# Performance work log

Hardware: AMD Instinct MI355X
Metric: run time of the kernel (lower is better)

Reference implementation:

```python
import jax, jax.numpy as jnp
import numpy as np

IN_F = 4096
OUT_F = 4096
Q_LEVELS = 16  # 4-bit


def setup_inputs() -> dict:
    key = jax.random.key(0)
    k = jax.random.split(key, 7)
    input = jax.random.normal(k[0], (4, 128, IN_F), dtype=jnp.float32)
    qweight = jax.random.randint(k[1], (OUT_F, IN_F), 0, Q_LEVELS, dtype=jnp.int32)
    scales = jax.random.uniform(k[2], (OUT_F, 1), dtype=jnp.float32)
    zeros = jax.random.uniform(k[3], (OUT_F, 1), dtype=jnp.float32)
    outlier = jax.random.uniform(k[4], (OUT_F, IN_F), dtype=jnp.float32)
    grad_updates = jax.random.normal(k[5], (OUT_F, IN_F), dtype=jnp.float32)
    bias = jax.random.normal(k[6], (OUT_F,), dtype=jnp.float32)
    return {"input": input, "qweight": qweight, "scales": scales,
            "zeros": zeros, "outlier": outlier,
            "grad_updates": grad_updates, "bias": bias}


def reference(input, qweight, scales, zeros, outlier, grad_updates, bias):
    # dequantize: affine per-output-row quantization -> dense weight [out, in]
    weight = (qweight.astype(jnp.float32) - zeros) * scales
    # sparse outlier correction (densified), scaled by learned GradUpdates
    weight = weight + outlier * grad_updates
    # F.linear: y = x @ W^T + b
    return jnp.einsum('bsi,oi->bso', input, weight) + bias
```

## Files before the change

kernel.cpp:

```cpp
#include <hip/hip_runtime.h>
#include <stdint.h>

#define IN_F   4096
#define OUT_F  4096
#define M_TOT  512
#define KT     (IN_F / 32)
#define BN     64
#define BK     64
#define KSPLIT 4
#define KPB    (IN_F / KSPLIT)
#define NITER  (KPB / BK)

typedef unsigned short u16;
typedef __bf16 bf16x8 __attribute__((ext_vector_type(8)));
typedef float  f32x4  __attribute__((ext_vector_type(4)));
typedef int    i32x4  __attribute__((ext_vector_type(4)));
typedef float  fv4    __attribute__((ext_vector_type(4)));

__device__ __forceinline__ u16 f2bf(float x) {
    unsigned u = __float_as_uint(x);
    u += 0x7FFFu + ((u >> 16) & 1u);
    return (u16)(u >> 16);
}

__global__ void pack_a_kernel(const float* __restrict__ in, u16* __restrict__ aws) {
    int t    = blockIdx.x * blockDim.x + threadIdx.x;
    int lane = t & 63;
    int kt   = (t >> 6) & (KT - 1);
    int mt   = t >> 13;
    int m = mt * 16 + (lane & 15);
    int k = kt * 32 + ((lane >> 4) << 3);
    const float* src = in + (size_t)m * IN_F + k;
    float4 a0 = *(const float4*)src;
    float4 a1 = *(const float4*)(src + 4);
    union { u16 u[8]; uint4 v; } pk;
    pk.u[0]=f2bf(a0.x); pk.u[1]=f2bf(a0.y); pk.u[2]=f2bf(a0.z); pk.u[3]=f2bf(a0.w);
    pk.u[4]=f2bf(a1.x); pk.u[5]=f2bf(a1.y); pk.u[6]=f2bf(a1.z); pk.u[7]=f2bf(a1.w);
    *(uint4*)(aws + (size_t)t * 8) = pk.v;
}

__global__ __launch_bounds__(1024, 4) void qlinear_kernel(
    const u16*   __restrict__ aws,
    const int*   __restrict__ qw,
    const float* __restrict__ scales,
    const float* __restrict__ zeros,
    const float* __restrict__ outlier,
    const float* __restrict__ grad,
    float*       __restrict__ part)
{
    __shared__ __align__(16) u16 Bsh[2][8 * 64 * 8];

    const int tid  = threadIdx.x;
    const int lane = tid & 63;
    const int wv   = tid >> 6;

    const int nblk = blockIdx.x >> 2;
    const int kq   = blockIdx.x & 3;
    const int n0   = nblk * BN;
    const int k0   = kq * KPB;

    const int srow = tid >> 4;
    const int schk = tid & 15;
    const int orow = n0 + srow;
    const float sr = scales[orow];
    const float c0 = -zeros[orow] * sr;
    const size_t sg = (size_t)orow * IN_F + k0 + schk * 4;
    const int sks   = schk >> 3;
    const int squad = (schk >> 1) & 3;
    const int j0    = (schk & 1) * 4;
    const int snf   = srow >> 4;
    const int slane = (srow & 15) | (squad << 4);
    const int doff  = ((sks * 4 + snf) * 64 + slane) * 8 + j0;

    i32x4 qb[2]; fv4 ob[2], gb[2];
    auto ld = [&](int it) {
        int s = it & 1;
        size_t off = sg + (size_t)it * BK;
        qb[s] = __builtin_nontemporal_load((const i32x4*)(qw      + off));
        ob[s] = __builtin_nontemporal_load((const fv4*)  (outlier + off));
        gb[s] = __builtin_nontemporal_load((const fv4*)  (grad    + off));
    };
    auto st = [&](int it) {
        int s = it & 1;
        union { u16 u[4]; uint2 v; } pk;
        pk.u[0] = f2bf(fmaf((float)qb[s].x, sr, fmaf(ob[s].x, gb[s].x, c0)));
        pk.u[1] = f2bf(fmaf((float)qb[s].y, sr, fmaf(ob[s].y, gb[s].y, c0)));
        pk.u[2] = f2bf(fmaf((float)qb[s].z, sr, fmaf(ob[s].z, gb[s].z, c0)));
        pk.u[3] = f2bf(fmaf((float)qb[s].w, sr, fmaf(ob[s].w, gb[s].w, c0)));
        *(uint2*)(&Bsh[it & 1][doff]) = pk.v;
    };

    const u16* abase = aws + ((size_t)(wv * 2) * KT + kq * (KPB / 32)) * 512
                           + (size_t)lane * 8;

    f32x4 acc[2][4] = {};

    ld(0);
    ld(1);
    st(0);
    asm volatile("s_waitcnt lgkmcnt(0)" ::: "memory");
    __builtin_amdgcn_s_barrier();

    for (int it = 0; it < NITER; ++it) {
        bf16x8 af[2][2];
        #pragma unroll
        for (int ks = 0; ks < 2; ++ks)
            #pragma unroll
            for (int mf = 0; mf < 2; ++mf)
                af[ks][mf] = *(const bf16x8*)(abase + ((size_t)mf * KT + it * 2 + ks) * 512);

        if (it + 2 < NITER) ld(it + 2);

        const u16* bb = &Bsh[it & 1][0];
        #pragma unroll
        for (int ks = 0; ks < 2; ++ks) {
            bf16x8 bfr[4];
            #pragma unroll
            for (int nf = 0; nf < 4; ++nf)
                bfr[nf] = *(const bf16x8*)(bb + (((ks * 4 + nf) * 64) + lane) * 8);
            #pragma unroll
            for (int mf = 0; mf < 2; ++mf)
                #pragma unroll
                for (int nf = 0; nf < 4; ++nf)
                    acc[mf][nf] = __builtin_amdgcn_mfma_f32_16x16x32_bf16(
                        af[ks][mf], bfr[nf], acc[mf][nf], 0, 0, 0);
        }

        if (it + 1 < NITER) st(it + 1);

        asm volatile("s_waitcnt lgkmcnt(0)" ::: "memory");
        __builtin_amdgcn_s_barrier();
    }

    float* pout = part + (size_t)kq * (M_TOT * OUT_F);
    const int cm0 = wv * 32 + ((lane >> 4) << 2);
    const int cn  = n0 + (lane & 15);
    #pragma unroll
    for (int mf = 0; mf < 2; ++mf)
        #pragma unroll
        for (int nf = 0; nf < 4; ++nf)
            #pragma unroll
            for (int r = 0; r < 4; ++r)
                __builtin_nontemporal_store(
                    acc[mf][nf][r],
                    pout + (size_t)(cm0 + mf * 16 + r) * OUT_F + cn + nf * 16);
}

__global__ void reduce_kernel(const fv4* __restrict__ part,
                              const fv4* __restrict__ bias,
                              fv4* __restrict__ out) {
    int idx = blockIdx.x * blockDim.x + threadIdx.x;
    fv4 s = bias[idx & (OUT_F / 4 - 1)];
    const int STRIDE = M_TOT * OUT_F / 4;
    #pragma unroll
    for (int k = 0; k < KSPLIT; ++k) {
        fv4 p = __builtin_nontemporal_load(part + (size_t)k * STRIDE + idx);
        s += p;
    }
    out[idx] = s;
}

extern "C" void kernel_launch(void* const* d_in, const int* in_sizes, int n_in,
                              void* d_out, int out_size, void* d_ws, size_t ws_size,
                              hipStream_t stream) {
    const float* input   = (const float*)d_in[0];
    const int*   qweight = (const int*)  d_in[1];
    const float* scales  = (const float*)d_in[2];
    const float* zeros   = (const float*)d_in[3];
    const float* outlier = (const float*)d_in[4];
    const float* grad    = (const float*)d_in[5];
    const float* bias    = (const float*)d_in[6];
    float* out = (float*)d_out;

    u16*   aws  = (u16*)d_ws;
    float* part = (float*)((char*)d_ws + (4u << 20));

    pack_a_kernel<<<(M_TOT * IN_F / 8) / 256, 256, 0, stream>>>(input, aws);
    qlinear_kernel<<<(OUT_F / BN) * KSPLIT, 1024, 0, stream>>>(
        aws, qweight, scales, zeros, outlier, grad, part);
    reduce_kernel<<<(M_TOT * OUT_F / 4) / 256, 256, 0, stream>>>(
        (const fv4*)part, (const fv4*)bias, (fv4*)out);
}
```

Measured before the change: 215.9 us.

## Halve output tile width to double block count and per-CU occupancy

Reduces the N tile from 64 to 32 columns, doubling the number of blocks and raising the launch-bounds occupancy hint so two blocks can share a CU. The per-thread weight loads shrink to 2-element vectors and the shared-memory B tile and accumulator set halve. The aim is more concurrent waves to hide the latency of the fp32/int32 weight streams. In exchange, each block rereads the full activation slice, doubling A-operand traffic, and loads become narrower.

```diff
diff --git a/kernel.cpp b/kernel.cpp
--- a/kernel.cpp
+++ b/kernel.cpp
@@ -5,7 +5,7 @@
 #define OUT_F  4096
 #define M_TOT  512
 #define KT     (IN_F / 32)
-#define BN     64
+#define BN     32
 #define BK     64
 #define KSPLIT 4
 #define KPB    (IN_F / KSPLIT)
@@ -14,7 +14,8 @@
 typedef unsigned short u16;
 typedef __bf16 bf16x8 __attribute__((ext_vector_type(8)));
 typedef float  f32x4  __attribute__((ext_vector_type(4)));
-typedef int    i32x4  __attribute__((ext_vector_type(4)));
+typedef float  f32x2  __attribute__((ext_vector_type(2)));
+typedef int    i32x2  __attribute__((ext_vector_type(2)));
 typedef float  fv4    __attribute__((ext_vector_type(4)));
 
 __device__ __forceinline__ u16 f2bf(float x) {
@@ -39,7 +40,7 @@
     *(uint4*)(aws + (size_t)t * 8) = pk.v;
 }
 
-__global__ __launch_bounds__(1024, 4) void qlinear_kernel(
+__global__ __launch_bounds__(1024, 8) void qlinear_kernel(
     const u16*   __restrict__ aws,
     const int*   __restrict__ qw,
     const float* __restrict__ scales,
@@ -48,7 +49,7 @@
     const float* __restrict__ grad,
     float*       __restrict__ part)
 {
-    __shared__ __align__(16) u16 Bsh[2][8 * 64 * 8];
+    __shared__ __align__(16) u16 Bsh[2][4 * 64 * 8];
 
     const int tid  = threadIdx.x;
     const int lane = tid & 63;
@@ -59,41 +60,39 @@
     const int n0   = nblk * BN;
     const int k0   = kq * KPB;
 
-    const int srow = tid >> 4;
-    const int schk = tid & 15;
+    const int srow = tid >> 5;
+    const int schk = tid & 31;
     const int orow = n0 + srow;
     const float sr = scales[orow];
     const float c0 = -zeros[orow] * sr;
-    const size_t sg = (size_t)orow * IN_F + k0 + schk * 4;
-    const int sks   = schk >> 3;
-    const int squad = (schk >> 1) & 3;
-    const int j0    = (schk & 1) * 4;
+    const size_t sg = (size_t)orow * IN_F + k0 + schk * 2;
+    const int sks   = schk >> 4;
+    const int squad = (schk >> 2) & 3;
+    const int j0    = (schk & 3) * 2;
     const int snf   = srow >> 4;
     const int slane = (srow & 15) | (squad << 4);
-    const int doff  = ((sks * 4 + snf) * 64 + slane) * 8 + j0;
+    const int doff  = ((sks * 2 + snf) * 64 + slane) * 8 + j0;
 
-    i32x4 qb[2]; fv4 ob[2], gb[2];
+    i32x2 qb[2]; f32x2 ob[2], gb[2];
     auto ld = [&](int it) {
         int s = it & 1;
         size_t off = sg + (size_t)it * BK;
-        qb[s] = __builtin_nontemporal_load((const i32x4*)(qw      + off));
-        ob[s] = __builtin_nontemporal_load((const fv4*)  (outlier + off));
-        gb[s] = __builtin_nontemporal_load((const fv4*)  (grad    + off));
+        qb[s] = __builtin_nontemporal_load((const i32x2*)(qw      + off));
+        ob[s] = __builtin_nontemporal_load((const f32x2*)(outlier + off));
+        gb[s] = __builtin_nontemporal_load((const f32x2*)(grad    + off));
     };
     auto st = [&](int it) {
         int s = it & 1;
-        union { u16 u[4]; uint2 v; } pk;
+        union { u16 u[2]; unsigned v; } pk;
         pk.u[0] = f2bf(fmaf((float)qb[s].x, sr, fmaf(ob[s].x, gb[s].x, c0)));
         pk.u[1] = f2bf(fmaf((float)qb[s].y, sr, fmaf(ob[s].y, gb[s].y, c0)));
-        pk.u[2] = f2bf(fmaf((float)qb[s].z, sr, fmaf(ob[s].z, gb[s].z, c0)));
-        pk.u[3] = f2bf(fmaf((float)qb[s].w, sr, fmaf(ob[s].w, gb[s].w, c0)));
-        *(uint2*)(&Bsh[it & 1][doff]) = pk.v;
+        *(unsigned*)(&Bsh[it & 1][doff]) = pk.v;
     };
 
     const u16* abase = aws + ((size_t)(wv * 2) * KT + kq * (KPB / 32)) * 512
                            + (size_t)lane * 8;
 
-    f32x4 acc[2][4] = {};
+    f32x4 acc[2][2] = {};
 
     ld(0);
     ld(1);
@@ -114,16 +113,12 @@
         const u16* bb = &Bsh[it & 1][0];
         #pragma unroll
         for (int ks = 0; ks < 2; ++ks) {
-            bf16x8 bfr[4];
-            #pragma unroll
-            for (int nf = 0; nf < 4; ++nf)
-                bfr[nf] = *(const bf16x8*)(bb + (((ks * 4 + nf) * 64) + lane) * 8);
-            #pragma unroll
-            for (int mf = 0; mf < 2; ++mf)
-                #pragma unroll
-                for (int nf = 0; nf < 4; ++nf)
-                    acc[mf][nf] = __builtin_amdgcn_mfma_f32_16x16x32_bf16(
-                        af[ks][mf], bfr[nf], acc[mf][nf], 0, 0, 0);
+            bf16x8 bf0 = *(const bf16x8*)(bb + (((ks * 2 + 0) * 64) + lane) * 8);
+            bf16x8 bf1 = *(const bf16x8*)(bb + (((ks * 2 + 1) * 64) + lane) * 8);
+            acc[0][0] = __builtin_amdgcn_mfma_f32_16x16x32_bf16(af[ks][0], bf0, acc[0][0], 0, 0, 0);
+            acc[0][1] = __builtin_amdgcn_mfma_f32_16x16x32_bf16(af[ks][0], bf1, acc[0][1], 0, 0, 0);
+            acc[1][0] = __builtin_amdgcn_mfma_f32_16x16x32_bf16(af[ks][1], bf0, acc[1][0], 0, 0, 0);
+            acc[1][1] = __builtin_amdgcn_mfma_f32_16x16x32_bf16(af[ks][1], bf1, acc[1][1], 0, 0, 0);
         }
 
         if (it + 1 < NITER) st(it + 1);
@@ -138,7 +133,7 @@
     #pragma unroll
     for (int mf = 0; mf < 2; ++mf)
         #pragma unroll
-        for (int nf = 0; nf < 4; ++nf)
+        for (int nf = 0; nf < 2; ++nf)
             #pragma unroll
             for (int r = 0; r < 4; ++r)
                 __builtin_nontemporal_store(
```

After: 257.1 us. +19.1%, slower.

## Split weight dequantization into a separate bf16 pass and swizzle LDS layout

Applied to the files above, without the earlier changes.

Moves the dequantization of qweight, outlier and grad into its own full-occupancy elementwise kernel that writes a bf16 weight buffer to workspace. The GEMM kernel then streams only bf16 weights and stores them directly to LDS. An XOR swizzle on the LDS store and load offsets is added to reduce bank conflicts. This unfuses the dequant from the GEMM, adding a write and re-read of a 32MB bf16 buffer in exchange for better bandwidth saturation in the dequant stage and a lighter GEMM inner loop.

```diff
diff --git a/kernel.cpp b/kernel.cpp
--- a/kernel.cpp
+++ b/kernel.cpp
@@ -39,13 +39,40 @@
     *(uint4*)(aws + (size_t)t * 8) = pk.v;
 }
 
-__global__ __launch_bounds__(1024, 4) void qlinear_kernel(
-    const u16*   __restrict__ aws,
+__global__ __launch_bounds__(256) void dequant_kernel(
     const int*   __restrict__ qw,
     const float* __restrict__ scales,
     const float* __restrict__ zeros,
     const float* __restrict__ outlier,
     const float* __restrict__ grad,
+    u16*         __restrict__ wws)
+{
+    int t = blockIdx.x * blockDim.x + threadIdx.x;
+    int row = t >> 9;
+    const float sr = scales[row];
+    const float c0 = -zeros[row] * sr;
+    size_t e = (size_t)t * 8;
+    i32x4 q0 = __builtin_nontemporal_load((const i32x4*)(qw      + e));
+    i32x4 q1 = __builtin_nontemporal_load((const i32x4*)(qw      + e + 4));
+    fv4   o0 = __builtin_nontemporal_load((const fv4*)  (outlier + e));
+    fv4   o1 = __builtin_nontemporal_load((const fv4*)  (outlier + e + 4));
+    fv4   g0 = __builtin_nontemporal_load((const fv4*)  (grad    + e));
+    fv4   g1 = __builtin_nontemporal_load((const fv4*)  (grad    + e + 4));
+    union { u16 u[8]; uint4 v; } pk;
+    pk.u[0] = f2bf(fmaf((float)q0.x, sr, fmaf(o0.x, g0.x, c0)));
+    pk.u[1] = f2bf(fmaf((float)q0.y, sr, fmaf(o0.y, g0.y, c0)));
+    pk.u[2] = f2bf(fmaf((float)q0.z, sr, fmaf(o0.z, g0.z, c0)));
+    pk.u[3] = f2bf(fmaf((float)q0.w, sr, fmaf(o0.w, g0.w, c0)));
+    pk.u[4] = f2bf(fmaf((float)q1.x, sr, fmaf(o1.x, g1.x, c0)));
+    pk.u[5] = f2bf(fmaf((float)q1.y, sr, fmaf(o1.y, g1.y, c0)));
+    pk.u[6] = f2bf(fmaf((float)q1.z, sr, fmaf(o1.z, g1.z, c0)));
+    pk.u[7] = f2bf(fmaf((float)q1.w, sr, fmaf(o1.w, g1.w, c0)));
+    *(uint4*)(wws + e) = pk.v;
+}
+
+__global__ __launch_bounds__(1024, 4) void qlinear_kernel(
+    const u16*   __restrict__ aws,
+    const u16*   __restrict__ wws,
     float*       __restrict__ part)
 {
     __shared__ __align__(16) u16 Bsh[2][8 * 64 * 8];
@@ -62,32 +89,21 @@
     const int srow = tid >> 4;
     const int schk = tid & 15;
     const int orow = n0 + srow;
-    const float sr = scales[orow];
-    const float c0 = -zeros[orow] * sr;
     const size_t sg = (size_t)orow * IN_F + k0 + schk * 4;
     const int sks   = schk >> 3;
     const int squad = (schk >> 1) & 3;
     const int j0    = (schk & 1) * 4;
     const int snf   = srow >> 4;
     const int slane = (srow & 15) | (squad << 4);
-    const int doff  = ((sks * 4 + snf) * 64 + slane) * 8 + j0;
-
-    i32x4 qb[2]; fv4 ob[2], gb[2];
+    const int doff  = ((((sks * 4 + snf) * 64 + slane) * 8 + j0) ^ (squad << 3));
+    const int rsw   = ((lane >> 4) & 3) << 3;
+
+    uint2 wb[2];
     auto ld = [&](int it) {
-        int s = it & 1;
-        size_t off = sg + (size_t)it * BK;
-        qb[s] = __builtin_nontemporal_load((const i32x4*)(qw      + off));
-        ob[s] = __builtin_nontemporal_load((const fv4*)  (outlier + off));
-        gb[s] = __builtin_nontemporal_load((const fv4*)  (grad    + off));
+        wb[it & 1] = *(const uint2*)(wws + sg + (size_t)it * BK);
     };
     auto st = [&](int it) {
-        int s = it & 1;
-        union { u16 u[4]; uint2 v; } pk;
-        pk.u[0] = f2bf(fmaf((float)qb[s].x, sr, fmaf(ob[s].x, gb[s].x, c0)));
-        pk.u[1] = f2bf(fmaf((float)qb[s].y, sr, fmaf(ob[s].y, gb[s].y, c0)));
-        pk.u[2] = f2bf(fmaf((float)qb[s].z, sr, fmaf(ob[s].z, gb[s].z, c0)));
-        pk.u[3] = f2bf(fmaf((float)qb[s].w, sr, fmaf(ob[s].w, gb[s].w, c0)));
-        *(uint2*)(&Bsh[it & 1][doff]) = pk.v;
+        *(uint2*)(&Bsh[it & 1][doff]) = wb[it & 1];
     };
 
     const u16* abase = aws + ((size_t)(wv * 2) * KT + kq * (KPB / 32)) * 512
@@ -117,7 +133,7 @@
             bf16x8 bfr[4];
             #pragma unroll
             for (int nf = 0; nf < 4; ++nf)
-                bfr[nf] = *(const bf16x8*)(bb + (((ks * 4 + nf) * 64) + lane) * 8);
+                bfr[nf] = *(const bf16x8*)(bb + (((((ks * 4 + nf) * 64) + lane) * 8) ^ rsw));
             #pragma unroll
             for (int mf = 0; mf < 2; ++mf)
                 #pragma unroll
@@ -173,11 +189,13 @@
     float* out = (float*)d_out;
 
     u16*   aws  = (u16*)d_ws;
-    float* part = (float*)((char*)d_ws + (4u << 20));
+    u16*   wws  = (u16*)((char*)d_ws + (4u << 20));
+    float* part = (float*)((char*)d_ws + (36u << 20));
 
     pack_a_kernel<<<(M_TOT * IN_F / 8) / 256, 256, 0, stream>>>(input, aws);
-    qlinear_kernel<<<(OUT_F / BN) * KSPLIT, 1024, 0, stream>>>(
-        aws, qweight, scales, zeros, outlier, grad, part);
+    dequant_kernel<<<(OUT_F * (size_t)IN_F / 8) / 256, 256, 0, stream>>>(
+        qweight, scales, zeros, outlier, grad, wws);
+    qlinear_kernel<<<(OUT_F / BN) * KSPLIT, 1024, 0, stream>>>(aws, wws, part);
     reduce_kernel<<<(M_TOT * OUT_F / 4) / 256, 256, 0, stream>>>(
         (const fv4*)part, (const fv4*)bias, (fv4*)out);
 }
```

Measured after the change: 230.3 us. 6.7% more time.
